# Performance work log

Measured on AMD Instinct MI355X. Metric: run time of the kernel, lower is better.

The kernel has to match this reference:

```python
import jax, jax.numpy as jnp
import numpy as np

SAMPLE_RATE = 16000
M = 10          # welch averaging window (frames)
R = 30          # long-term window (frames)
EPS = 1e-5
WIN_LEN = 25    # source bug: ms value used as window length in samples


def _hamming_sq_sum(n):
    # torch.hamming_window(n, periodic=True): 0.54 - 0.46*cos(2*pi*k/n)
    k = np.arange(n)
    w = 0.54 - 0.46 * np.cos(2.0 * np.pi * k / n)
    return np.float32((w ** 2).sum())


def _windowed_mean(x, w):
    """y[:, i, :] = mean(x[:, max(0, i-w):i, :]) for i>=1, y[:,0,:]=0.
    Vectorized via prefix sums: replaces the per-frame Python loop."""
    B, T, F = x.shape
    c = jnp.cumsum(x, axis=1)
    c = jnp.concatenate([jnp.zeros((B, 1, F), x.dtype), c], axis=1)  # c[:, i] = sum of first i frames
    idx = jnp.arange(T)
    lo = jnp.maximum(idx - w, 0)
    cnt = jnp.minimum(idx, w).astype(x.dtype)            # window length per frame (0 at i=0)
    mean = (c[:, idx] - c[:, lo]) / jnp.maximum(cnt, 1)[None, :, None]
    return mean  # mean[:,0,:] == 0 since numerator is 0 there


def setup_inputs() -> dict:
    key = jax.random.key(0)
    x = jax.random.normal(key, (32, 3000, 201, 2), dtype=jnp.float32)
    return {"x": x}


def reference(x) -> jnp.ndarray:
    B, T, F, _ = x.shape
    # speechbrain spectral_magnitude (power=1): power spectrum re^2 + im^2
    spectr = jnp.sum(x * x, axis=-1) / M                         # (B, T, F)
    # welch scaling: /fs * sum(window^2), interior bins doubled
    scale = jnp.ones((F,), x.dtype).at[1:-1].set(2.0)
    s = spectr * (_hamming_sq_sum(WIN_LEN) / SAMPLE_RATE) * scale[None, None, :]
    welch = _windowed_mean(s, M)                                 # (B, T, F)
    # long-term geometric and arithmetic means over R frames of the welch spectrum
    t0 = (jnp.arange(T) == 0)[None, :, None]
    geo = jnp.exp(_windowed_mean(jnp.log(welch + EPS), R)) - EPS
    gm = jnp.where(t0, 0.0, geo) + EPS                           # frame 0 forced to 0 (as in source)
    am = _windowed_mean(welch, R) + EPS
    flatness = -jnp.sum(jnp.log10(gm / am), axis=-1, keepdims=True)  # (B, T, 1)
    return flatness
```

## Files before the change

kernel.cpp:

```cpp
#include <hip/hip_runtime.h>


constexpr int TT = 3000;
constexpr int FF = 201;
constexpr int BB = 32;
constexpr int W1 = 10;
constexpr int W2 = 30;
constexpr int HALO = 40;
constexpr int LTILE = 60;
constexpr int NT = 50;
#define EPSV 1e-5f
#define CSCALE (9.935f / 160000.0f)
#define LOG10_2 0.3010299956639812f

#define SUPERGROUP(DYN)                                                        \
  {                                                                            \
            \
    float a0 = 0.f, a1 = 0.f, a2 = 0.f;                                        \
    _Pragma("unroll") for (int j = 0; j < W2; ++j) {                           \
      a0 += w_ring[j]; a1 += l_ring[j];                                        \
    }                                                                          \
    _Pragma("unroll") for (int j = 0; j < W1; ++j) a2 += s_ring[j];            \
    wsum = a0; lsum = a1; ssum = a2;                                           \
    _Pragma("unroll") for (int g = 0; g < 6; ++g) {                            \
                                                   \
      _Pragma("unroll") for (int j = 0; j < 5; ++j) {                          \
        int tt = min(tstart + kbase + m0 + (g + 1) * 5 + j, tmax);             \
        nxt[j] = xb[(size_t)tt * FF + f];                                      \
      }                                                                        \
      float rr[5];                                                             \
      _Pragma("unroll") for (int j = 0; j < 5; ++j) {                          \
        const int fr = g * 5 + j;                \
        const int slot30 = fr;                                                 \
        const int slot10 = fr % 10;                                            \
        int t = t0 + m0 + fr;                                                  \
        float inv10, inv30;                                                    \
        if (DYN) {                                                             \
          inv10 = 1.0f / (float)max(min(t, W1), 1);                            \
          inv30 = 1.0f / (float)max(min(t, W2), 1);                            \
        } else {                                                               \
          inv10 = 0.1f;                                                        \
          inv30 = (1.0f / 30.0f);                                              \
        }                                                                      \
        float welch = ssum * inv10;                                            \
        float lw = __log2f(welch + EPSV);                                      \
        float am = fmaf(wsum, inv30, EPSV);                                    \
        float la = __log2f(am);                                                \
        rr[j] = (la - lsum * inv30) * LOG10_2;                                 \
        wsum += welch - w_ring[slot30]; w_ring[slot30] = welch;                \
        lsum += lw - l_ring[slot30];    l_ring[slot30] = lw;                   \
        float sv = fmaf(cur[j].x, cur[j].x, cur[j].y * cur[j].y) * cs;         \
        ssum += sv - s_ring[slot10]; s_ring[slot10] = sv;                      \
      }                                                                        \
                  \
      _Pragma("unroll") for (int off = 32; off >= 1; off >>= 1) {              \
        _Pragma("unroll") for (int j = 0; j < 5; ++j)                          \
            rr[j] += __shfl_xor(rr[j], off, 64);                               \
      }                                                                        \
      if (lane == 0) {                                                         \
        _Pragma("unroll") for (int j = 0; j < 5; ++j)                          \
            part[wv][m0 + g * 5 + j] = rr[j];                                  \
      }                                                                        \
      _Pragma("unroll") for (int j = 0; j < 5; ++j) cur[j] = nxt[j];           \
    }                                                                          \
    m0 += 30;                                                                  \
  }

__global__ __launch_bounds__(256, 4)
void ltsf_kernel(const float2* __restrict__ x, float* __restrict__ out) {
  const int tid = threadIdx.x;
  const int tile = blockIdx.x;
  const int b = blockIdx.y;
  const int t0 = tile * LTILE;
  const bool first = (tile == 0);
  const int tstart = first ? 0 : (t0 - HALO);
  const int lane = tid & 63;
  const int wv = tid >> 6;

  const int f = (tid < FF) ? tid : (FF - 1);
  float cs = (tid < FF) ? ((tid == 0 || tid == FF - 1) ? 1.0f : 2.0f) : 0.0f;
  cs *= CSCALE;

  const float2* xb = x + (size_t)b * TT * FF;
  const int tmax = t0 + LTILE - 1;

  __shared__ float part[4][LTILE];

  float s_ring[W1], w_ring[W2], l_ring[W2];
#pragma unroll
  for (int j = 0; j < W1; ++j) s_ring[j] = 0.f;
#pragma unroll
  for (int j = 0; j < W2; ++j) { w_ring[j] = 0.f; l_ring[j] = 0.f; }
  float ssum = 0.f, wsum = 0.f, lsum = 0.f;

  float2 cur[5], nxt[5];

#pragma unroll
  for (int j = 0; j < 5; ++j) {
    int tt = min(tstart + j, tmax);
    cur[j] = xb[(size_t)tt * FF + f];
  }

  const int kbase = first ? 0 : HALO;
  int m0 = 0;

  if (!first) {
#pragma unroll
    for (int g = 0; g < 2; ++g) {
#pragma unroll
      for (int j = 0; j < 5; ++j) {
        int tt = min(tstart + (g + 1) * 5 + j, tmax);
        nxt[j] = xb[(size_t)tt * FF + f];
      }
#pragma unroll
      for (int j = 0; j < 5; ++j) {
        float sv = fmaf(cur[j].x, cur[j].x, cur[j].y * cur[j].y) * cs;
        ssum += sv;
        s_ring[g * 5 + j] = sv;
      }
#pragma unroll
      for (int j = 0; j < 5; ++j) cur[j] = nxt[j];
    }
#pragma unroll
    for (int g = 0; g < 6; ++g) {
#pragma unroll
      for (int j = 0; j < 5; ++j) {
        int tt = min(tstart + 15 + g * 5 + j, tmax);
        nxt[j] = xb[(size_t)tt * FF + f];
      }
#pragma unroll
      for (int j = 0; j < 5; ++j) {
        const int fr = g * 5 + j;
        float welch = ssum * 0.1f;
        float lw = __log2f(welch + EPSV);
        wsum += welch; w_ring[fr] = welch;
        lsum += lw;    l_ring[fr] = lw;
        float sv = fmaf(cur[j].x, cur[j].x, cur[j].y * cur[j].y) * cs;
        ssum += sv - s_ring[fr % 10];
        s_ring[fr % 10] = sv;
      }
#pragma unroll
      for (int j = 0; j < 5; ++j) cur[j] = nxt[j];
    }
  }

  if (first) {
    SUPERGROUP(true);
    SUPERGROUP(false);
  } else {
    SUPERGROUP(false);
    SUPERGROUP(false);
  }

  __syncthreads();
  if (tid < LTILE) {
    float v = part[0][tid] + part[1][tid] + part[2][tid] + part[3][tid];
    if (first && tid == 0) v = 0.f;
    out[(size_t)b * TT + t0 + tid] = v;
  }
}

extern "C" void kernel_launch(void* const* d_in, const int* in_sizes, int n_in,
                              void* d_out, int out_size, void* d_ws, size_t ws_size,
                              hipStream_t stream) {
  const float2* x = (const float2*)d_in[0];
  float* out = (float*)d_out;
  dim3 grid(NT, BB);
  ltsf_kernel<<<grid, 256, 0, stream>>>(x, out);
}
```

Measured before the change: 223.9 us.

## Drop log ring, recompute old log, ping-pong loads, shorter shuffle reduction

Removes the 30-entry log ring buffer and instead recomputes the outgoing log term from the stored welch value, cutting register use so launch bounds can rise to 5 blocks per SIMD. Loads switch to pointer-bumped ping-pong buffers without per-element clamping, and the per-supergroup ring re-summation is removed. The cross-lane shuffle reduction stops at offset 2, leaving 4 partials per wave that are written to a float4 shared slot and summed at the end. In exchange it does an extra log per frame, and the unclamped prefetch may read past the tile (last group reloads the same rows via TERM). Removing the periodic re-summation may also let float drift accumulate in the running sums.

```diff
diff --git a/kernel.cpp b/kernel.cpp
--- a/kernel.cpp
+++ b/kernel.cpp
@@ -13,27 +13,17 @@
 #define CSCALE (9.935f / 160000.0f)
 #define LOG10_2 0.3010299956639812f
 
-#define SUPERGROUP(DYN)                                                        \
+#define SUPERGROUP(DYN, TERM)                                                  \
   {                                                                            \
-            \
-    float a0 = 0.f, a1 = 0.f, a2 = 0.f;                                        \
-    _Pragma("unroll") for (int j = 0; j < W2; ++j) {                           \
-      a0 += w_ring[j]; a1 += l_ring[j];                                        \
-    }                                                                          \
-    _Pragma("unroll") for (int j = 0; j < W1; ++j) a2 += s_ring[j];            \
-    wsum = a0; lsum = a1; ssum = a2;                                           \
     _Pragma("unroll") for (int g = 0; g < 6; ++g) {                            \
-                                                   \
-      _Pragma("unroll") for (int j = 0; j < 5; ++j) {                          \
-        int tt = min(tstart + kbase + m0 + (g + 1) * 5 + j, tmax);             \
-        nxt[j] = xb[(size_t)tt * FF + f];                                      \
-      }                                                                        \
+      float2* cb = (g & 1) ? b1 : b0;          \
+      float2* nb = (g & 1) ? b0 : b1;                                          \
+      const float2* pn = ((TERM) && g == 5) ? pf : (pf + 5 * FF);              \
+      _Pragma("unroll") for (int j = 0; j < 5; ++j) nb[j] = pn[j * FF];        \
       float rr[5];                                                             \
       _Pragma("unroll") for (int j = 0; j < 5; ++j) {                          \
-        const int fr = g * 5 + j;                \
-        const int slot30 = fr;                                                 \
-        const int slot10 = fr % 10;                                            \
-        int t = t0 + m0 + fr;                                                  \
+        const int fr = g * 5 + j;        \
+        const int t = t0 + m0 + fr;                                            \
         float inv10, inv30;                                                    \
         if (DYN) {                                                             \
           inv10 = 1.0f / (float)max(min(t, W1), 1);                            \
@@ -47,26 +37,31 @@
         float am = fmaf(wsum, inv30, EPSV);                                    \
         float la = __log2f(am);                                                \
         rr[j] = (la - lsum * inv30) * LOG10_2;                                 \
-        wsum += welch - w_ring[slot30]; w_ring[slot30] = welch;                \
-        lsum += lw - l_ring[slot30];    l_ring[slot30] = lw;                   \
-        float sv = fmaf(cur[j].x, cur[j].x, cur[j].y * cur[j].y) * cs;         \
-        ssum += sv - s_ring[slot10]; s_ring[slot10] = sv;                      \
+        float wold = w_ring[fr];                                               \
+        if (DYN) lsum += lw;                   \
+        else     lsum += lw - __log2f(wold + EPSV);    \
+        wsum += welch - wold;                                                  \
+        w_ring[fr] = welch;                                                    \
+        float sv = fmaf(cb[j].x, cb[j].x, cb[j].y * cb[j].y) * cs;             \
+        ssum += sv - s_ring[fr % 10];                                          \
+        s_ring[fr % 10] = sv;                                                  \
       }                                                                        \
-                  \
-      _Pragma("unroll") for (int off = 32; off >= 1; off >>= 1) {              \
+        \
+      _Pragma("unroll") for (int off = 16; off >= 2; off >>= 1) {              \
         _Pragma("unroll") for (int j = 0; j < 5; ++j)                          \
             rr[j] += __shfl_xor(rr[j], off, 64);                               \
       }                                                                        \
-      if (lane == 0) {                                                         \
+      if ((lane & 30) == 0) {                                                  \
+        const int p = (lane & 1) | ((lane >> 4) & 2);                          \
         _Pragma("unroll") for (int j = 0; j < 5; ++j)                          \
-            part[wv][m0 + g * 5 + j] = rr[j];                                  \
+            ((float*)&part[wv][m0 + g * 5 + j])[p] = rr[j];                    \
       }                                                                        \
-      _Pragma("unroll") for (int j = 0; j < 5; ++j) cur[j] = nxt[j];           \
+      pf = pn;                                                                 \
     }                                                                          \
     m0 += 30;                                                                  \
   }
 
-__global__ __launch_bounds__(256, 4)
+__global__ __launch_bounds__(256, 5)
 void ltsf_kernel(const float2* __restrict__ x, float* __restrict__ out) {
   const int tid = threadIdx.x;
   const int tile = blockIdx.x;
@@ -82,79 +77,76 @@
   cs *= CSCALE;
 
   const float2* xb = x + (size_t)b * TT * FF;
-  const int tmax = t0 + LTILE - 1;
 
-  __shared__ float part[4][LTILE];
+  __shared__ float4 part[4][LTILE];
 
-  float s_ring[W1], w_ring[W2], l_ring[W2];
+  float s_ring[W1], w_ring[W2];
 #pragma unroll
   for (int j = 0; j < W1; ++j) s_ring[j] = 0.f;
 #pragma unroll
-  for (int j = 0; j < W2; ++j) { w_ring[j] = 0.f; l_ring[j] = 0.f; }
+  for (int j = 0; j < W2; ++j) w_ring[j] = 0.f;
   float ssum = 0.f, wsum = 0.f, lsum = 0.f;
 
-  float2 cur[5], nxt[5];
+  float2 b0[5], b1[5];
+  const float2* pf = xb + (size_t)tstart * FF + f;
 
 #pragma unroll
-  for (int j = 0; j < 5; ++j) {
-    int tt = min(tstart + j, tmax);
-    cur[j] = xb[(size_t)tt * FF + f];
-  }
+  for (int j = 0; j < 5; ++j) b0[j] = pf[j * FF];
 
-  const int kbase = first ? 0 : HALO;
   int m0 = 0;
 
   if (!first) {
 #pragma unroll
     for (int g = 0; g < 2; ++g) {
+      float2* cb = (g & 1) ? b1 : b0;
+      float2* nb = (g & 1) ? b0 : b1;
+      const float2* pn = pf + 5 * FF;
+#pragma unroll
+      for (int j = 0; j < 5; ++j) nb[j] = pn[j * FF];
 #pragma unroll
       for (int j = 0; j < 5; ++j) {
-        int tt = min(tstart + (g + 1) * 5 + j, tmax);
-        nxt[j] = xb[(size_t)tt * FF + f];
-      }
-#pragma unroll
-      for (int j = 0; j < 5; ++j) {
-        float sv = fmaf(cur[j].x, cur[j].x, cur[j].y * cur[j].y) * cs;
+        float sv = fmaf(cb[j].x, cb[j].x, cb[j].y * cb[j].y) * cs;
         ssum += sv;
         s_ring[g * 5 + j] = sv;
       }
-#pragma unroll
-      for (int j = 0; j < 5; ++j) cur[j] = nxt[j];
+      pf = pn;
     }
 #pragma unroll
     for (int g = 0; g < 6; ++g) {
+      float2* cb = (g & 1) ? b1 : b0;
+      float2* nb = (g & 1) ? b0 : b1;
+      const float2* pn = pf + 5 * FF;
 #pragma unroll
-      for (int j = 0; j < 5; ++j) {
-        int tt = min(tstart + 15 + g * 5 + j, tmax);
-        nxt[j] = xb[(size_t)tt * FF + f];
-      }
+      for (int j = 0; j < 5; ++j) nb[j] = pn[j * FF];
 #pragma unroll
       for (int j = 0; j < 5; ++j) {
         const int fr = g * 5 + j;
         float welch = ssum * 0.1f;
         float lw = __log2f(welch + EPSV);
         wsum += welch; w_ring[fr] = welch;
-        lsum += lw;    l_ring[fr] = lw;
-        float sv = fmaf(cur[j].x, cur[j].x, cur[j].y * cur[j].y) * cs;
+        lsum += lw;
+        float sv = fmaf(cb[j].x, cb[j].x, cb[j].y * cb[j].y) * cs;
         ssum += sv - s_ring[fr % 10];
         s_ring[fr % 10] = sv;
       }
-#pragma unroll
-      for (int j = 0; j < 5; ++j) cur[j] = nxt[j];
+      pf = pn;
     }
   }
 
   if (first) {
-    SUPERGROUP(true);
-    SUPERGROUP(false);
+    SUPERGROUP(true, false);
+    SUPERGROUP(false, true);
   } else {
-    SUPERGROUP(false);
-    SUPERGROUP(false);
+    SUPERGROUP(false, false);
+    SUPERGROUP(false, true);
   }
 
   __syncthreads();
   if (tid < LTILE) {
-    float v = part[0][tid] + part[1][tid] + part[2][tid] + part[3][tid];
+    float4 v0 = part[0][tid], v1 = part[1][tid];
+    float4 v2 = part[2][tid], v3 = part[3][tid];
+    float v = ((v0.x + v0.y) + (v0.z + v0.w)) + ((v1.x + v1.y) + (v1.z + v1.w)) +
+              ((v2.x + v2.y) + (v2.z + v2.w)) + ((v3.x + v3.y) + (v3.z + v3.w));
     if (first && tid == 0) v = 0.f;
     out[(size_t)b * TT + t0 + tid] = v;
   }
```

Measured after the change: 284.3 us. +27.0%, slower.
